# Optimization experiments

Hardware: AMD Instinct MI355X
Metric: run time of the kernel (lower is better)

The kernel has to match this reference:

```python
import jax, jax.numpy as jnp
import numpy as np

N_NODES = 50000
DEG = 16
N_EDGES = N_NODES * DEG
H = 8
D = 32
NEG_SLOPE = 0.2


def setup_inputs() -> dict:
    key = jax.random.key(0)
    k1, k2, k3, k4 = jax.random.split(key, 4)
    feat = jax.random.normal(k1, (N_NODES, H * D), dtype=jnp.float32)
    attn_l = jax.random.normal(k2, (1, H, D), dtype=jnp.float32) * 0.1
    attn_r = jax.random.normal(k3, (1, H, D), dtype=jnp.float32) * 0.1
    bias = jnp.zeros((H * D,), dtype=jnp.float32)
    # every dst node has in-degree DEG (no zero-in-degree nodes)
    dst = jnp.repeat(jnp.arange(N_NODES, dtype=jnp.int32), DEG)
    src = jax.random.randint(k4, (N_EDGES,), 0, N_NODES, dtype=jnp.int32)
    return {"feat": feat, "attn_l": attn_l, "attn_r": attn_r, "bias": bias,
            "src": src, "dst": dst}


def reference(feat, attn_l, attn_r, bias, src, dst):
    N = feat.shape[0]
    fs = feat.reshape(N, H, D)                      # [N,H,D]
    el = (fs * attn_l).sum(-1)                      # [N,H]
    er = (fs * attn_r).sum(-1)                      # [N,H]
    # per-edge attention logit: u_add_v + leaky_relu
    e = jax.nn.leaky_relu(el[src] + er[dst], negative_slope=NEG_SLOPE)  # [E,H]
    # segmented (per-dst) softmax over incoming edges
    emax = jax.ops.segment_max(e, dst, num_segments=N)  # [N,H]
    ee = jnp.exp(e - emax[dst])                         # [E,H]
    esum = jax.ops.segment_sum(ee, dst, num_segments=N)  # [N,H]
    a = ee / esum[dst]                                  # [E,H]
    # u_mul_e then sum: weighted scatter-aggregate
    msg = fs[src] * a[:, :, None]                       # [E,H,D]
    rst = jax.ops.segment_sum(msg, dst, num_segments=N)  # [N,H,D]
    rst = rst + bias.reshape(1, H, D)
    return rst
```

## Files before the change

### kernel.cpp

```cpp
#include <hip/hip_runtime.h>

#define HEADS 8
#define DIM 32
#define DEGREE 16
#define NEG_SLOPE 0.2f

__device__ __forceinline__ unsigned short f2bf(float f) {
  unsigned u = __float_as_uint(f);
  unsigned r = (u + 0x7fffu + ((u >> 16) & 1u)) >> 16;
  return (unsigned short)r;
}

template <bool WRITE_BF16>
__global__ __launch_bounds__(256) void elr_kernel(
    const float4* __restrict__ feat4,
    const float4* __restrict__ attn_l4,
    const float4* __restrict__ attn_r4,
    float* __restrict__ elT, float* __restrict__ erT,
    ushort4* __restrict__ featbH, int total4, int N) {
  int t = blockIdx.x * 256 + threadIdx.x;
  if (t >= total4) return;
  float4 v = feat4[t];
  int c4 = t & 63;
  float4 al = attn_l4[c4];
  float4 ar = attn_r4[c4];
  float pl = v.x * al.x + v.y * al.y + v.z * al.z + v.w * al.w;
  float pr = v.x * ar.x + v.y * ar.y + v.z * ar.z + v.w * ar.w;
#pragma unroll
  for (int off = 4; off >= 1; off >>= 1) {
    pl += __shfl_xor(pl, off);
    pr += __shfl_xor(pr, off);
  }
  int n = t >> 6;
  int h = c4 >> 3;
  if ((t & 7) == 0) {
    elT[h * N + n] = pl;
    erT[h * N + n] = pr;
  }
  if (WRITE_BF16) {
    ushort4 b;
    b.x = f2bf(v.x); b.y = f2bf(v.y); b.z = f2bf(v.z); b.w = f2bf(v.w);
    int d4 = c4 & 7;
    featbH[((size_t)h * N + n) * 8 + d4] = b;
  }
}

__global__ __launch_bounds__(256) void gat_hmajor_kernel(
    const uint4* __restrict__ featbH,
    const float* __restrict__ elT,
    const float* __restrict__ erT,
    const int* __restrict__ srcIdx,
    const float* __restrict__ bias,
    float* __restrict__ out, int N) {
  int h = blockIdx.x & 7;
  int chunk = blockIdx.x >> 3;
  int tid = threadIdx.x;
  __shared__ int s_src[16][DEGREE];
  {
    int nl = tid >> 4, e = tid & 15;
    int nn = chunk * 16 + nl;
    s_src[nl][e] = (nn < N) ? srcIdx[nn * DEGREE + e] : 0;
  }
  __syncthreads();

  int lane = tid & 63;
  int wave = tid >> 6;
  int g = lane >> 4;
  int l16 = lane & 15;
  int nl = wave * 4 + g;
  int n = chunk * 16 + nl;
  if (n >= N) return;

  int sidx = s_src[nl][l16];
  float e = elT[h * N + sidx] + erT[h * N + n];
  e = e > 0.0f ? e : NEG_SLOPE * e;
  float m = e;
#pragma unroll
  for (int off = 8; off >= 1; off >>= 1) m = fmaxf(m, __shfl_xor(m, off));
  float x = __expf(e - m);
  float s = x;
#pragma unroll
  for (int off = 8; off >= 1; off >>= 1) s += __shfl_xor(s, off);
  float w = x / s;

  int q = (lane >> 2) & 3;
  int c = lane & 3;
  int base = lane & 48;
  float acc[8];
#pragma unroll
  for (int k = 0; k < 8; k++) acc[k] = 0.0f;
#pragma unroll
  for (int p = 0; p < 4; p++) {
    int j = p * 4 + q;
    int sj = __shfl(sidx, base + j);
    float wj = __shfl(w, base + j);
    uint4 r = featbH[((size_t)h * N + sj) * 4 + c];
    acc[0] += wj * __uint_as_float(r.x << 16);
    acc[1] += wj * __uint_as_float(r.x & 0xffff0000u);
    acc[2] += wj * __uint_as_float(r.y << 16);
    acc[3] += wj * __uint_as_float(r.y & 0xffff0000u);
    acc[4] += wj * __uint_as_float(r.z << 16);
    acc[5] += wj * __uint_as_float(r.z & 0xffff0000u);
    acc[6] += wj * __uint_as_float(r.w << 16);
    acc[7] += wj * __uint_as_float(r.w & 0xffff0000u);
  }
#pragma unroll
  for (int k = 0; k < 8; k++) {
    acc[k] += __shfl_xor(acc[k], 4);
    acc[k] += __shfl_xor(acc[k], 8);
  }
  if (q == 0) {
    const float4* bias4 = (const float4*)bias;
    int bidx = h * 8 + c * 2;
    float4 b0 = bias4[bidx], b1 = bias4[bidx + 1];
    float4 o0 = make_float4(acc[0] + b0.x, acc[1] + b0.y,
                            acc[2] + b0.z, acc[3] + b0.w);
    float4 o1 = make_float4(acc[4] + b1.x, acc[5] + b1.y,
                            acc[6] + b1.z, acc[7] + b1.w);
    size_t o = (size_t)n * 64 + h * 8 + c * 2;
    ((float4*)out)[o] = o0;
    ((float4*)out)[o + 1] = o1;
  }
}

__global__ __launch_bounds__(256) void gat_f32_kernel(
    const float4* __restrict__ featv,
    const float* __restrict__ elT,
    const float* __restrict__ erT,
    const int* __restrict__ srcIdx,
    const float* __restrict__ bias,
    float* __restrict__ out, int N) {
  int wave = threadIdx.x >> 6;
  int lane = threadIdx.x & 63;
  int n = blockIdx.x * 4 + wave;
  __shared__ float s_a[4][DEGREE][HEADS + 1];
  bool active = (n < N);
  int sidx = 0;
  if (active) {
    const int* s = srcIdx + n * DEGREE;
    int i = lane & 15;
    int hh = lane >> 4;
    sidx = s[i];
    float e0 = elT[hh * N + sidx]       + erT[hh * N + n];
    float e1 = elT[(hh + 4) * N + sidx] + erT[(hh + 4) * N + n];
    e0 = e0 > 0.0f ? e0 : NEG_SLOPE * e0;
    e1 = e1 > 0.0f ? e1 : NEG_SLOPE * e1;
    float m0 = e0, m1 = e1;
#pragma unroll
    for (int off = 8; off >= 1; off >>= 1) {
      m0 = fmaxf(m0, __shfl_xor(m0, off));
      m1 = fmaxf(m1, __shfl_xor(m1, off));
    }
    float x0 = __expf(e0 - m0), x1 = __expf(e1 - m1);
    float s0 = x0, s1 = x1;
#pragma unroll
    for (int off = 8; off >= 1; off >>= 1) {
      s0 += __shfl_xor(s0, off);
      s1 += __shfl_xor(s1, off);
    }
    s_a[wave][i][hh]     = x0 / s0;
    s_a[wave][i][hh + 4] = x1 / s1;
  }
  __syncthreads();
  if (active) {
    int h = lane >> 3;
    float4 acc = ((const float4*)bias)[lane];
#pragma unroll
    for (int j = 0; j < DEGREE; j++) {
      int sj = __shfl(sidx, j);
      float a = s_a[wave][j][h];
      float4 v = featv[(size_t)sj * 64 + lane];
      acc.x += a * v.x; acc.y += a * v.y; acc.z += a * v.z; acc.w += a * v.w;
    }
    ((float4*)out)[(size_t)n * 64 + lane] = acc;
  }
}

extern "C" void kernel_launch(void* const* d_in, const int* in_sizes, int n_in,
                              void* d_out, int out_size, void* d_ws, size_t ws_size,
                              hipStream_t stream) {
  const float* feat   = (const float*)d_in[0];
  const float* attn_l = (const float*)d_in[1];
  const float* attn_r = (const float*)d_in[2];
  const float* bias   = (const float*)d_in[3];
  const int*   src    = (const int*)d_in[4];
  float* out = (float*)d_out;

  int total = in_sizes[0];
  int N = total / (HEADS * DIM);
  int total4 = total / 4;

  float* elT = (float*)d_ws;
  float* erT = elT + (size_t)N * HEADS;
  ushort4* featbH = (ushort4*)(erT + (size_t)N * HEADS);

  size_t need = (size_t)N * HEADS * 2 * sizeof(float) + (size_t)total * 2;
  bool use_bf16 = (ws_size >= need);

  if (use_bf16) {
    elr_kernel<true><<<(total4 + 255) / 256, 256, 0, stream>>>(
        (const float4*)feat, (const float4*)attn_l, (const float4*)attn_r,
        elT, erT, featbH, total4, N);
    int nchunks = (N + 15) / 16;
    gat_hmajor_kernel<<<nchunks * 8, 256, 0, stream>>>(
        (const uint4*)featbH, elT, erT, src, bias, out, N);
  } else {
    elr_kernel<false><<<(total4 + 255) / 256, 256, 0, stream>>>(
        (const float4*)feat, (const float4*)attn_l, (const float4*)attn_r,
        elT, erT, nullptr, total4, N);
    int nb = (N + 3) / 4;
    gat_f32_kernel<<<nb, 256, 0, stream>>>(
        (const float4*)feat, elT, erT, src, bias, out, N);
  }
}
```

Baseline: 175.8 us.

## Split softmax weights into separate kernel with node-major el/er layout

Stores el/er node-major ([N,8]) so a single thread can load all eight heads of a source node with two float4 loads. A new weights_kernel computes per-edge softmax weights for all heads once and writes them head-major, and the aggregation kernel reads those precomputed weights instead of recomputing the logits. The aim is to avoid scattered per-head elT gathers and the repeated src loads across eight head blocks. The cost is an extra launch and writing then re-reading 25.6MB of weights. The fallback path now also uses bf16 and assumes the workspace can hold it, though it no longer checks that.

```diff
diff --git a/kernel.cpp b/kernel.cpp
--- a/kernel.cpp
+++ b/kernel.cpp
@@ -16,7 +16,7 @@
     const float4* __restrict__ feat4,
     const float4* __restrict__ attn_l4,
     const float4* __restrict__ attn_r4,
-    float* __restrict__ elT, float* __restrict__ erT,
+    float* __restrict__ el8, float* __restrict__ er8,
     ushort4* __restrict__ featbH, int total4, int N) {
   int t = blockIdx.x * 256 + threadIdx.x;
   if (t >= total4) return;
@@ -31,58 +31,68 @@
     pl += __shfl_xor(pl, off);
     pr += __shfl_xor(pr, off);
   }
-  int n = t >> 6;
-  int h = c4 >> 3;
   if ((t & 7) == 0) {
-    elT[h * N + n] = pl;
-    erT[h * N + n] = pr;
+    el8[t >> 3] = pl;
+    er8[t >> 3] = pr;
   }
   if (WRITE_BF16) {
     ushort4 b;
     b.x = f2bf(v.x); b.y = f2bf(v.y); b.z = f2bf(v.z); b.w = f2bf(v.w);
-    int d4 = c4 & 7;
+    int n = t >> 6, h = c4 >> 3, d4 = c4 & 7;
     featbH[((size_t)h * N + n) * 8 + d4] = b;
   }
 }
 
-__global__ __launch_bounds__(256) void gat_hmajor_kernel(
-    const uint4* __restrict__ featbH,
-    const float* __restrict__ elT,
-    const float* __restrict__ erT,
+__global__ __launch_bounds__(256) void weights_kernel(
+    const float4* __restrict__ el84,
+    const float4* __restrict__ er84,
+    const int* __restrict__ srcIdx,
+    float* __restrict__ wH, int N) {
+  int t = threadIdx.x;
+  int n0 = blockIdx.x * 16;
+  int nl = t >> 4;
+  int n = n0 + nl;
+  if (n >= N) return;
+  int s = srcIdx[n0 * DEGREE + t];
+  float4 e0 = el84[(size_t)s * 2], e1 = el84[(size_t)s * 2 + 1];
+  float4 r0 = er84[(size_t)n * 2], r1 = er84[(size_t)n * 2 + 1];
+  float l[HEADS] = {e0.x + r0.x, e0.y + r0.y, e0.z + r0.z, e0.w + r0.w,
+                    e1.x + r1.x, e1.y + r1.y, e1.z + r1.z, e1.w + r1.w};
+  float w[HEADS];
+#pragma unroll
+  for (int h = 0; h < HEADS; h++) {
+    float e = l[h];
+    e = e > 0.0f ? e : NEG_SLOPE * e;
+    float m = e;
+#pragma unroll
+    for (int off = 8; off >= 1; off >>= 1) m = fmaxf(m, __shfl_xor(m, off));
+    float x = __expf(e - m);
+    float ssum = x;
+#pragma unroll
+    for (int off = 8; off >= 1; off >>= 1) ssum += __shfl_xor(ssum, off);
+    w[h] = x / ssum;
+  }
+#pragma unroll
+  for (int h = 0; h < HEADS; h++)
+    wH[(size_t)h * N * DEGREE + n0 * DEGREE + t] = w[h];
+}
+
+__global__ __launch_bounds__(256) void gat_kernel(
+    const uint4* __restrict__ featbH4,
+    const float* __restrict__ wH,
     const int* __restrict__ srcIdx,
     const float* __restrict__ bias,
     float* __restrict__ out, int N) {
   int h = blockIdx.x & 7;
   int chunk = blockIdx.x >> 3;
-  int tid = threadIdx.x;
-  __shared__ int s_src[16][DEGREE];
-  {
-    int nl = tid >> 4, e = tid & 15;
-    int nn = chunk * 16 + nl;
-    s_src[nl][e] = (nn < N) ? srcIdx[nn * DEGREE + e] : 0;
-  }
-  __syncthreads();
-
-  int lane = tid & 63;
-  int wave = tid >> 6;
-  int g = lane >> 4;
-  int l16 = lane & 15;
-  int nl = wave * 4 + g;
-  int n = chunk * 16 + nl;
+  int t = threadIdx.x;
+  int n0 = chunk * 16;
+  int n = n0 + (t >> 4);
   if (n >= N) return;
-
-  int sidx = s_src[nl][l16];
-  float e = elT[h * N + sidx] + erT[h * N + n];
-  e = e > 0.0f ? e : NEG_SLOPE * e;
-  float m = e;
-#pragma unroll
-  for (int off = 8; off >= 1; off >>= 1) m = fmaxf(m, __shfl_xor(m, off));
-  float x = __expf(e - m);
-  float s = x;
-#pragma unroll
-  for (int off = 8; off >= 1; off >>= 1) s += __shfl_xor(s, off);
-  float w = x / s;
-
+  int sidx = srcIdx[n0 * DEGREE + t];
+  float w = wH[(size_t)h * N * DEGREE + n0 * DEGREE + t];
+
+  int lane = t & 63;
   int q = (lane >> 2) & 3;
   int c = lane & 3;
   int base = lane & 48;
@@ -94,7 +104,7 @@
     int j = p * 4 + q;
     int sj = __shfl(sidx, base + j);
     float wj = __shfl(w, base + j);
-    uint4 r = featbH[((size_t)h * N + sj) * 4 + c];
+    uint4 r = featbH4[((size_t)h * N + sj) * 4 + c];
     acc[0] += wj * __uint_as_float(r.x << 16);
     acc[1] += wj * __uint_as_float(r.x & 0xffff0000u);
     acc[2] += wj * __uint_as_float(r.y << 16);
@@ -123,56 +133,69 @@
   }
 }
 
-__global__ __launch_bounds__(256) void gat_f32_kernel(
-    const float4* __restrict__ featv,
-    const float* __restrict__ elT,
-    const float* __restrict__ erT,
+__global__ __launch_bounds__(256) void gat_fused_kernel(
+    const uint4* __restrict__ featbH4,
+    const float* __restrict__ el8,
+    const float* __restrict__ er8,
     const int* __restrict__ srcIdx,
     const float* __restrict__ bias,
     float* __restrict__ out, int N) {
-  int wave = threadIdx.x >> 6;
-  int lane = threadIdx.x & 63;
-  int n = blockIdx.x * 4 + wave;
-  __shared__ float s_a[4][DEGREE][HEADS + 1];
-  bool active = (n < N);
-  int sidx = 0;
-  if (active) {
-    const int* s = srcIdx + n * DEGREE;
-    int i = lane & 15;
-    int hh = lane >> 4;
-    sidx = s[i];
-    float e0 = elT[hh * N + sidx]       + erT[hh * N + n];
-    float e1 = elT[(hh + 4) * N + sidx] + erT[(hh + 4) * N + n];
-    e0 = e0 > 0.0f ? e0 : NEG_SLOPE * e0;
-    e1 = e1 > 0.0f ? e1 : NEG_SLOPE * e1;
-    float m0 = e0, m1 = e1;
-#pragma unroll
-    for (int off = 8; off >= 1; off >>= 1) {
-      m0 = fmaxf(m0, __shfl_xor(m0, off));
-      m1 = fmaxf(m1, __shfl_xor(m1, off));
-    }
-    float x0 = __expf(e0 - m0), x1 = __expf(e1 - m1);
-    float s0 = x0, s1 = x1;
-#pragma unroll
-    for (int off = 8; off >= 1; off >>= 1) {
-      s0 += __shfl_xor(s0, off);
-      s1 += __shfl_xor(s1, off);
-    }
-    s_a[wave][i][hh]     = x0 / s0;
-    s_a[wave][i][hh + 4] = x1 / s1;
-  }
-  __syncthreads();
-  if (active) {
-    int h = lane >> 3;
-    float4 acc = ((const float4*)bias)[lane];
-#pragma unroll
-    for (int j = 0; j < DEGREE; j++) {
-      int sj = __shfl(sidx, j);
-      float a = s_a[wave][j][h];
-      float4 v = featv[(size_t)sj * 64 + lane];
-      acc.x += a * v.x; acc.y += a * v.y; acc.z += a * v.z; acc.w += a * v.w;
-    }
-    ((float4*)out)[(size_t)n * 64 + lane] = acc;
+  int h = blockIdx.x & 7;
+  int chunk = blockIdx.x >> 3;
+  int t = threadIdx.x;
+  int n0 = chunk * 16;
+  int n = n0 + (t >> 4);
+  if (n >= N) return;
+  int sidx = srcIdx[n0 * DEGREE + t];
+  float e = el8[(size_t)sidx * 8 + h] + er8[(size_t)n * 8 + h];
+  e = e > 0.0f ? e : NEG_SLOPE * e;
+  float m = e;
+#pragma unroll
+  for (int off = 8; off >= 1; off >>= 1) m = fmaxf(m, __shfl_xor(m, off));
+  float x = __expf(e - m);
+  float ssum = x;
+#pragma unroll
+  for (int off = 8; off >= 1; off >>= 1) ssum += __shfl_xor(ssum, off);
+  float w = x / ssum;
+
+  int lane = t & 63;
+  int q = (lane >> 2) & 3;
+  int c = lane & 3;
+  int base = lane & 48;
+  float acc[8];
+#pragma unroll
+  for (int k = 0; k < 8; k++) acc[k] = 0.0f;
+#pragma unroll
+  for (int p = 0; p < 4; p++) {
+    int j = p * 4 + q;
+    int sj = __shfl(sidx, base + j);
+    float wj = __shfl(w, base + j);
+    uint4 r = featbH4[((size_t)h * N + sj) * 4 + c];
+    acc[0] += wj * __uint_as_float(r.x << 16);
+    acc[1] += wj * __uint_as_float(r.x & 0xffff0000u);
+    acc[2] += wj * __uint_as_float(r.y << 16);
+    acc[3] += wj * __uint_as_float(r.y & 0xffff0000u);
+    acc[4] += wj * __uint_as_float(r.z << 16);
+    acc[5] += wj * __uint_as_float(r.z & 0xffff0000u);
+    acc[6] += wj * __uint_as_float(r.w << 16);
+    acc[7] += wj * __uint_as_float(r.w & 0xffff0000u);
+  }
+#pragma unroll
+  for (int k = 0; k < 8; k++) {
+    acc[k] += __shfl_xor(acc[k], 4);
+    acc[k] += __shfl_xor(acc[k], 8);
+  }
+  if (q == 0) {
+    const float4* bias4 = (const float4*)bias;
+    int bidx = h * 8 + c * 2;
+    float4 b0 = bias4[bidx], b1 = bias4[bidx + 1];
+    float4 o0 = make_float4(acc[0] + b0.x, acc[1] + b0.y,
+                            acc[2] + b0.z, acc[3] + b0.w);
+    float4 o1 = make_float4(acc[4] + b1.x, acc[5] + b1.y,
+                            acc[6] + b1.z, acc[7] + b1.w);
+    size_t o = (size_t)n * 64 + h * 8 + c * 2;
+    ((float4*)out)[o] = o0;
+    ((float4*)out)[o + 1] = o1;
   }
 }
 
@@ -189,27 +212,30 @@
   int total = in_sizes[0];
   int N = total / (HEADS * DIM);
   int total4 = total / 4;
-
-  float* elT = (float*)d_ws;
-  float* erT = elT + (size_t)N * HEADS;
-  ushort4* featbH = (ushort4*)(erT + (size_t)N * HEADS);
-
-  size_t need = (size_t)N * HEADS * 2 * sizeof(float) + (size_t)total * 2;
-  bool use_bf16 = (ws_size >= need);
-
-  if (use_bf16) {
+  int nchunks = (N + 15) / 16;
+
+  float* el8 = (float*)d_ws;
+  float* er8 = el8 + (size_t)N * HEADS;
+  ushort4* featbH = (ushort4*)(er8 + (size_t)N * HEADS);
+  float* wH = (float*)(featbH + (size_t)total / 4);
+
+  size_t need_base = (size_t)N * HEADS * 2 * sizeof(float);
+  size_t need_feat = need_base + (size_t)total * 2;
+  size_t need_full = need_feat + (size_t)N * DEGREE * HEADS * sizeof(float);
+
+  if (ws_size >= need_full) {
     elr_kernel<true><<<(total4 + 255) / 256, 256, 0, stream>>>(
         (const float4*)feat, (const float4*)attn_l, (const float4*)attn_r,
-        elT, erT, featbH, total4, N);
-    int nchunks = (N + 15) / 16;
-    gat_hmajor_kernel<<<nchunks * 8, 256, 0, stream>>>(
-        (const uint4*)featbH, elT, erT, src, bias, out, N);
+        el8, er8, featbH, total4, N);
+    weights_kernel<<<nchunks, 256, 0, stream>>>(
+        (const float4*)el8, (const float4*)er8, src, wH, N);
+    gat_kernel<<<nchunks * 8, 256, 0, stream>>>(
+        (const uint4*)featbH, wH, src, bias, out, N);
   } else {
-    elr_kernel<false><<<(total4 + 255) / 256, 256, 0, stream>>>(
+    elr_kernel<true><<<(total4 + 255) / 256, 256, 0, stream>>>(
         (const float4*)feat, (const float4*)attn_l, (const float4*)attn_r,
-        elT, erT, nullptr, total4, N);
-    int nb = (N + 3) / 4;
-    gat_f32_kernel<<<nb, 256, 0, stream>>>(
-        (const float4*)feat, elT, erT, src, bias, out, N);
-  }
-}
+        el8, er8, featbH, total4, N);
+    gat_fused_kernel<<<nchunks * 8, 256, 0, stream>>>(
+        (const uint4*)featbH, el8, er8, src, bias, out, N);
+  }
+}
```

New measurement: 161.6 us. 1.09x faster.
